# Optimization experiments

Measured on AMD Instinct MI355X. Metric: run time of the kernel, lower is better.

The kernel has to match this reference:

```python
import jax, jax.numpy as jnp
import numpy as np

CHEBY = 3  # max_degree / number of Chebyshev polynomial orders
IN_F, OUT_F = 64, 64
B, N = 32, 2048


def setup_inputs() -> dict:
    key = jax.random.key(0)
    k1, k2, k3, k4, k5 = jax.random.split(key, 5)
    stdv = 1.0 / np.sqrt(OUT_F)
    stdv2 = 1.0  # 1/sqrt(K.size(1)) = 1/sqrt(1)
    x = jax.random.normal(k1, (B, N, IN_F), dtype=jnp.float32)
    adj = jax.random.uniform(k2, (B, N, N), dtype=jnp.float32)
    weight = jax.random.uniform(k3, (IN_F, OUT_F), minval=-stdv, maxval=stdv, dtype=jnp.float32)
    K = jax.random.uniform(k4, (CHEBY, 1), minval=-stdv2, maxval=stdv2, dtype=jnp.float32)
    bias = jax.random.uniform(k5, (OUT_F,), minval=-stdv, maxval=stdv, dtype=jnp.float32)
    return {"x": x, "adj": adj, "weight": weight, "K": K, "bias": bias}


def chebyshev_stack(x, adj, max_degree):
    # T_0 = x, T_1 = A x, T_k = 2 A T_{k-1} - T_{k-2}; stack along new last axis
    Ts = [x]
    if max_degree > 1:
        Ts.append(jnp.einsum('bnm,bmf->bnf', adj, x))
    for _ in range(2, max_degree):
        Ts.append(2.0 * jnp.einsum('bnm,bmf->bnf', adj, Ts[-1]) - Ts[-2])
    return jnp.stack(Ts, axis=-1)  # [B, N, F, K]


def reference(x, adj, weight, K, bias):
    support = chebyshev_stack(x, adj, CHEBY)            # [B, N, F, K]
    combined = jnp.einsum('bnfk,ko->bnf', support, K)   # K-weighted sum -> [B, N, F]
    out = jnp.einsum('bnf,fo->bno', combined, weight) + bias
    return out
```

## Files before the change

kernel.cpp:

```cpp
#include <hip/hip_runtime.h>
#include <stdint.h>

#define NN 2048
#define FF 64
#define NB 32

typedef __attribute__((ext_vector_type(8))) short bf16x8;
typedef __attribute__((ext_vector_type(4))) float f32x4;

__device__ __forceinline__ uint16_t f2bf(float f) {
  uint32_t u = __builtin_bit_cast(uint32_t, f);
  return (uint16_t)((u + 0x7FFFu + ((u >> 16) & 1u)) >> 16);
}
__device__ __forceinline__ float bf2f(uint16_t h) {
  uint32_t u = ((uint32_t)h) << 16;
  return __builtin_bit_cast(float, u);
}

__global__ void k_prep(const float* __restrict__ W, uint16_t* __restrict__ Wt) {
  int t = threadIdx.x;
  for (int i = 0; i < 16; ++i) {
    int idx = t * 16 + i;
    int k = idx >> 6, f = idx & 63;
    Wt[f * 64 + k] = f2bf(W[idx]);
  }
}

__global__ __launch_bounds__(256) void k_xw(const float* __restrict__ x,
                                            const uint16_t* __restrict__ Wt,
                                            uint16_t* __restrict__ xw,
                                            uint16_t* __restrict__ xwT) {
  __shared__ short As[64 * 72];
  int bid = blockIdx.x;
  int b = bid >> 5;
  int n0 = (bid & 31) * 64;
  int t = threadIdx.x;
  const float* xb = x + ((size_t)b * NN + n0) * FF;
  for (int i = 0; i < 4; ++i) {
    int idx = t + i * 256;
    int r = idx >> 4, c = (idx & 15) * 4;
    float4 v = *(const float4*)(xb + r * FF + c);
    uint32_t p0 = f2bf(v.x) | ((uint32_t)f2bf(v.y) << 16);
    uint32_t p1 = f2bf(v.z) | ((uint32_t)f2bf(v.w) << 16);
    uint2 pv = {p0, p1};
    *(uint2*)&As[r * 72 + c] = pv;
  }
  __syncthreads();
  int lane = t & 63, wave = t >> 6;
  int l16 = lane & 15, quad = lane >> 4;
  f32x4 acc[4] = {};
  for (int ks = 0; ks < 2; ++ks) {
    bf16x8 a = *(const bf16x8*)&As[(wave * 16 + l16) * 72 + ks * 32 + quad * 8];
    for (int fi = 0; fi < 4; ++fi) {
      bf16x8 bq = *(const bf16x8*)(Wt + (fi * 16 + l16) * 64 + ks * 32 + quad * 8);
      acc[fi] = __builtin_amdgcn_mfma_f32_16x16x32_bf16(a, bq, acc[fi], 0, 0, 0);
    }
  }
  for (int fi = 0; fi < 4; ++fi)
    for (int r = 0; r < 4; ++r) {
      int n = n0 + wave * 16 + quad * 4 + r;
      int f = fi * 16 + l16;
      xw[((size_t)b * NN + n) * FF + f] = f2bf(acc[fi][r]);
    }
  __syncthreads();
  uint16_t* T = (uint16_t*)As;
  for (int fi = 0; fi < 4; ++fi)
    for (int r = 0; r < 4; ++r)
      T[(fi * 16 + l16) * 72 + wave * 16 + quad * 4 + r] = f2bf(acc[fi][r]);
  __syncthreads();
  int f = t >> 2, seg = t & 3;
  uint4 v0 = *(const uint4*)&T[f * 72 + seg * 16];
  uint4 v1 = *(const uint4*)&T[f * 72 + seg * 16 + 8];
  uint16_t* dp = xwT + ((size_t)b * FF + f) * NN + n0 + seg * 16;
  *(uint4*)dp = v0;
  *(uint4*)(dp + 8) = v1;
}

template <int EPI>
__global__ __launch_bounds__(256, 4) void k_gemm(const float* __restrict__ adj,
                                                 const uint16_t* __restrict__ Bt,
                                                 uint16_t* __restrict__ Yb,
                                                 uint16_t* __restrict__ YbT,
                                                 const uint16_t* __restrict__ xw,
                                                 const uint16_t* __restrict__ y1,
                                                 const float* __restrict__ Kc,
                                                 const float* __restrict__ bias,
                                                 float* __restrict__ out) {
  __shared__ short As[2][64 * 72];
  __shared__ short Bs[2][64 * 72];
  int bid = blockIdx.x;
  int b = bid & 31;
  int rt = bid >> 5;
  int row0 = rt << 6;
  int t = threadIdx.x;
  int lane = t & 63, wave = t >> 6;
  int l16 = lane & 15, quad = lane >> 4;
  int krot = ((b * 11) + rt * 7) & 31;
  const float* Ab = adj + (size_t)b * NN * NN + (size_t)row0 * NN;
  const uint16_t* Btb = Bt + (size_t)b * FF * NN;

  int ra[4], ca[4];
  for (int i = 0; i < 4; ++i) {
    int chunk = t + i * 256;
    ra[i] = chunk >> 4;
    ca[i] = (chunk & 15) * 4;
  }
  int fb[2], kb8[2];
  for (int j = 0; j < 2; ++j) {
    int chunk = t + j * 256;
    fb[j] = chunk >> 3;
    kb8[j] = (chunk & 7) * 8;
  }

  float4 areg[4];
  uint4 breg[2];
  {
    int kn = krot * 64;
    for (int i = 0; i < 4; ++i)
      areg[i] = *(const float4*)(Ab + (size_t)ra[i] * NN + kn + ca[i]);
    for (int j = 0; j < 2; ++j)
      breg[j] = *(const uint4*)(Btb + (size_t)fb[j] * NN + kn + kb8[j]);
  }

  f32x4 acc[4] = {};
  for (int it = 0; it < 32; ++it) {
    asm volatile("s_waitcnt vmcnt(0)" ::: "memory");
    int p = it & 1;
    for (int i = 0; i < 4; ++i) {
      float4 v = areg[i];
      uint32_t p0 = f2bf(v.x) | ((uint32_t)f2bf(v.y) << 16);
      uint32_t p1 = f2bf(v.z) | ((uint32_t)f2bf(v.w) << 16);
      uint2 pv = {p0, p1};
      *(uint2*)&As[p][ra[i] * 72 + ca[i]] = pv;
    }
    for (int j = 0; j < 2; ++j)
      *(uint4*)&Bs[p][fb[j] * 72 + kb8[j]] = breg[j];
    if (it + 1 < 32) {
      int kn = ((krot + it + 1) & 31) * 64;
      for (int i = 0; i < 4; ++i)
        areg[i] = *(const float4*)(Ab + (size_t)ra[i] * NN + kn + ca[i]);
      for (int j = 0; j < 2; ++j)
        breg[j] = *(const uint4*)(Btb + (size_t)fb[j] * NN + kn + kb8[j]);
    }
    asm volatile("s_waitcnt lgkmcnt(0)" ::: "memory");
    __builtin_amdgcn_s_barrier();
    for (int ks = 0; ks < 2; ++ks) {
      bf16x8 a = *(const bf16x8*)&As[p][(wave * 16 + l16) * 72 + ks * 32 + quad * 8];
      for (int fi = 0; fi < 4; ++fi) {
        bf16x8 bq = *(const bf16x8*)&Bs[p][(fi * 16 + l16) * 72 + ks * 32 + quad * 8];
        acc[fi] = __builtin_amdgcn_mfma_f32_16x16x32_bf16(a, bq, acc[fi], 0, 0, 0);
      }
    }
  }

  if (EPI == 0) {
    for (int fi = 0; fi < 4; ++fi)
      for (int r = 0; r < 4; ++r) {
        int n = row0 + wave * 16 + quad * 4 + r;
        int f = fi * 16 + l16;
        Yb[((size_t)b * NN + n) * FF + f] = f2bf(acc[fi][r]);
      }
    __syncthreads();
    uint16_t* T = (uint16_t*)&As[0][0];
    for (int fi = 0; fi < 4; ++fi)
      for (int r = 0; r < 4; ++r)
        T[(fi * 16 + l16) * 72 + wave * 16 + quad * 4 + r] = f2bf(acc[fi][r]);
    __syncthreads();
    int f = t >> 2, seg = t & 3;
    uint4 v0 = *(const uint4*)&T[f * 72 + seg * 16];
    uint4 v1 = *(const uint4*)&T[f * 72 + seg * 16 + 8];
    uint16_t* dp = YbT + ((size_t)b * FF + f) * NN + row0 + seg * 16;
    *(uint4*)dp = v0;
    *(uint4*)(dp + 8) = v1;
  } else {
    float ka = Kc[0] - Kc[2], kb = Kc[1], kc = 2.0f * Kc[2];
    for (int fi = 0; fi < 4; ++fi) {
      int f = fi * 16 + l16;
      float bv = bias[f];
      for (int r = 0; r < 4; ++r) {
        int n = row0 + wave * 16 + quad * 4 + r;
        size_t idx = ((size_t)b * NN + n) * FF + f;
        out[idx] = ka * bf2f(xw[idx]) + kb * bf2f(y1[idx]) + kc * acc[fi][r] + bv;
      }
    }
  }
}

extern "C" void kernel_launch(void* const* d_in, const int* in_sizes, int n_in,
                              void* d_out, int out_size, void* d_ws, size_t ws_size,
                              hipStream_t stream) {
  const float* x    = (const float*)d_in[0];
  const float* adj  = (const float*)d_in[1];
  const float* W    = (const float*)d_in[2];
  const float* K    = (const float*)d_in[3];
  const float* bias = (const float*)d_in[4];
  float* out = (float*)d_out;

  uint8_t* ws = (uint8_t*)d_ws;
  const size_t SZ = (size_t)NB * NN * FF * sizeof(uint16_t);
  uint16_t* xw_n = (uint16_t*)(ws);
  uint16_t* xwT  = (uint16_t*)(ws + SZ);
  uint16_t* y1_n = (uint16_t*)(ws + 2 * SZ);
  uint16_t* y1T  = (uint16_t*)(ws + 3 * SZ);
  uint16_t* Wt   = (uint16_t*)(ws + 4 * SZ);

  k_prep<<<dim3(1), dim3(256), 0, stream>>>(W, Wt);
  k_xw<<<dim3(1024), dim3(256), 0, stream>>>(x, Wt, xw_n, xwT);
  k_gemm<0><<<dim3(1024), dim3(256), 0, stream>>>(adj, xwT, y1_n, y1T, nullptr,
                                                  nullptr, nullptr, nullptr, nullptr);
  k_gemm<1><<<dim3(1024), dim3(256), 0, stream>>>(adj, y1T, nullptr, nullptr, xw_n,
                                                  y1_n, K, bias, out);
}
```

Baseline: 881.0 us.

## Fuse xw and both adjacency GEMMs into one cooperative kernel with grid syncs

```diff
diff --git a/kernel.cpp b/kernel.cpp
--- a/kernel.cpp
+++ b/kernel.cpp
@@ -1,5 +1,8 @@
 #include <hip/hip_runtime.h>
+#include <hip/hip_cooperative_groups.h>
 #include <stdint.h>
+
+namespace cg = cooperative_groups;
 
 #define NN 2048
 #define FF 64
@@ -26,11 +29,11 @@
   }
 }
 
-__global__ __launch_bounds__(256) void k_xw(const float* __restrict__ x,
-                                            const uint16_t* __restrict__ Wt,
-                                            uint16_t* __restrict__ xw,
-                                            uint16_t* __restrict__ xwT) {
-  __shared__ short As[64 * 72];
+__device__ __forceinline__ void phaseA(const float* __restrict__ x,
+                                       const uint16_t* __restrict__ Wt,
+                                       uint16_t* __restrict__ xw,
+                                       uint16_t* __restrict__ xwT,
+                                       short* As) {
   int bid = blockIdx.x;
   int b = bid >> 5;
   int n0 = (bid & 31) * 64;
@@ -76,18 +79,17 @@
   *(uint4*)(dp + 8) = v1;
 }
 
-template <int EPI>
-__global__ __launch_bounds__(256, 4) void k_gemm(const float* __restrict__ adj,
-                                                 const uint16_t* __restrict__ Bt,
-                                                 uint16_t* __restrict__ Yb,
-                                                 uint16_t* __restrict__ YbT,
-                                                 const uint16_t* __restrict__ xw,
-                                                 const uint16_t* __restrict__ y1,
-                                                 const float* __restrict__ Kc,
-                                                 const float* __restrict__ bias,
-                                                 float* __restrict__ out) {
-  __shared__ short As[2][64 * 72];
-  __shared__ short Bs[2][64 * 72];
+__device__ __forceinline__ void phaseG(int EPI,
+                                       const float* __restrict__ adj,
+                                       const uint16_t* __restrict__ Bt,
+                                       uint16_t* __restrict__ Yb,
+                                       uint16_t* __restrict__ YbT,
+                                       const uint16_t* __restrict__ xw,
+                                       const uint16_t* __restrict__ y1,
+                                       const float* __restrict__ Kc,
+                                       const float* __restrict__ bias,
+                                       float* __restrict__ out,
+                                       short (*As)[64 * 72], short (*Bs)[64 * 72]) {
   int bid = blockIdx.x;
   int b = bid & 31;
   int rt = bid >> 5;
@@ -186,6 +188,45 @@
   }
 }
 
+__global__ __launch_bounds__(256, 4) void k_fused(
+    const float* __restrict__ x, const float* __restrict__ adj,
+    const uint16_t* __restrict__ Wt, const float* __restrict__ Kc,
+    const float* __restrict__ bias, float* __restrict__ out,
+    uint16_t* __restrict__ xw, uint16_t* __restrict__ xwT,
+    uint16_t* __restrict__ y1, uint16_t* __restrict__ y1T) {
+  __shared__ short As[2][64 * 72];
+  __shared__ short Bs[2][64 * 72];
+  cg::grid_group grid = cg::this_grid();
+  phaseA(x, Wt, xw, xwT, &As[0][0]);
+  grid.sync();
+  phaseG(0, adj, xwT, y1, y1T, nullptr, nullptr, nullptr, nullptr, nullptr, As, Bs);
+  grid.sync();
+  phaseG(1, adj, y1T, nullptr, nullptr, xw, y1, Kc, bias, out, As, Bs);
+}
+
+__global__ __launch_bounds__(256) void k_xw(const float* __restrict__ x,
+                                            const uint16_t* __restrict__ Wt,
+                                            uint16_t* __restrict__ xw,
+                                            uint16_t* __restrict__ xwT) {
+  __shared__ short As[64 * 72];
+  phaseA(x, Wt, xw, xwT, As);
+}
+
+template <int EPI>
+__global__ __launch_bounds__(256, 4) void k_gemm(const float* __restrict__ adj,
+                                                 const uint16_t* __restrict__ Bt,
+                                                 uint16_t* __restrict__ Yb,
+                                                 uint16_t* __restrict__ YbT,
+                                                 const uint16_t* __restrict__ xw,
+                                                 const uint16_t* __restrict__ y1,
+                                                 const float* __restrict__ Kc,
+                                                 const float* __restrict__ bias,
+                                                 float* __restrict__ out) {
+  __shared__ short As[2][64 * 72];
+  __shared__ short Bs[2][64 * 72];
+  phaseG(EPI, adj, Bt, Yb, YbT, xw, y1, Kc, bias, out, As, Bs);
+}
+
 extern "C" void kernel_launch(void* const* d_in, const int* in_sizes, int n_in,
                               void* d_out, int out_size, void* d_ws, size_t ws_size,
                               hipStream_t stream) {
@@ -205,9 +246,17 @@
   uint16_t* Wt   = (uint16_t*)(ws + 4 * SZ);
 
   k_prep<<<dim3(1), dim3(256), 0, stream>>>(W, Wt);
-  k_xw<<<dim3(1024), dim3(256), 0, stream>>>(x, Wt, xw_n, xwT);
-  k_gemm<0><<<dim3(1024), dim3(256), 0, stream>>>(adj, xwT, y1_n, y1T, nullptr,
-                                                  nullptr, nullptr, nullptr, nullptr);
-  k_gemm<1><<<dim3(1024), dim3(256), 0, stream>>>(adj, y1T, nullptr, nullptr, xw_n,
-                                                  y1_n, K, bias, out);
-}
+
+  void* args[] = {(void*)&x,   (void*)&adj,  (void*)&Wt,   (void*)&K,
+                  (void*)&bias, (void*)&out, (void*)&xw_n, (void*)&xwT,
+                  (void*)&y1_n, (void*)&y1T};
+  hipError_t err = hipLaunchCooperativeKernel((const void*)k_fused, dim3(1024),
+                                              dim3(256), args, 0, stream);
+  if (err != hipSuccess) {
+    k_xw<<<dim3(1024), dim3(256), 0, stream>>>(x, Wt, xw_n, xwT);
+    k_gemm<0><<<dim3(1024), dim3(256), 0, stream>>>(adj, xwT, y1_n, y1T, nullptr,
+                                                    nullptr, nullptr, nullptr, nullptr);
+    k_gemm<1><<<dim3(1024), dim3(256), 0, stream>>>(adj, y1T, nullptr, nullptr, xw_n,
+                                                    y1_n, K, bias, out);
+  }
+}
```

After: 1.166 ms. 32.4% more time.
